# Kernel tuning notes

Measured on AMD Instinct MI355X. Metric: run time of the kernel, lower is better.

Reference implementation:

```python
import jax, jax.numpy as jnp
import numpy as np

DN = ('NCHW', 'OIHW', 'NCHW')

def _conv(x, w, pad):
    return jax.lax.conv_general_dilated(x, w, (1, 1), [(pad, pad), (pad, pad)], dimension_numbers=DN)

def setup_inputs() -> dict:
    key = jax.random.key(0)
    ks = jax.random.split(key, 6)
    B, Cin, Csh, H, W = 4, 128, 64, 512, 512
    s = lambda fan: (2.0 / fan) ** 0.5  # kaiming-ish scale
    return {
        'feature': jax.random.normal(ks[0], (B, Cin, H, W), jnp.float32),
        'w_shared': jax.random.normal(ks[1], (Csh, Cin, 3, 3), jnp.float32) * s(Cin * 9),
        'w_cls': jax.random.normal(ks[2], (2, Csh, 1, 1), jnp.float32) * s(Csh),
        'b_cls': jnp.zeros((2,), jnp.float32),
        'w_box': jax.random.normal(ks[3], (6, Csh, 1, 1), jnp.float32) * s(Csh),
        'b_box': jnp.zeros((6,), jnp.float32),
        'w_dir': jax.random.normal(ks[4], (8, Csh, 1, 1), jnp.float32) * s(Csh),
        'b_dir': jnp.zeros((8,), jnp.float32),
        'w_scr': jax.random.normal(ks[5], (4, Csh, 1, 1), jnp.float32) * s(Csh),
        'b_scr': jnp.zeros((4,), jnp.float32),
    }

def reference(feature, w_shared, w_cls, b_cls, w_box, b_box, w_dir, b_dir, w_scr, b_scr):
    # shared 3x3 conv (no bias) + ReLU -> [B, 64, H, W]
    x = jax.nn.relu(_conv(feature, w_shared, 1))
    bias = lambda b: b[None, :, None, None]
    cls = _conv(x, w_cls, 0) + bias(b_cls)                 # [B, n_cls+1, H, W]
    box = _conv(x, w_box, 0) + bias(b_box)                 # [B, 6, H, W]
    dr = _conv(x, w_dir, 0) + bias(b_dir)                  # [B, 8, H, W]
    scr = jax.nn.sigmoid(_conv(x, w_scr, 0) + bias(b_scr)) # sigmoid_keys=['scr']
    return jnp.concatenate([cls, box, dr, scr], axis=1)    # [B, 20, H, W]
```

## Files before the change

### kernel.cpp

```cpp
#include <hip/hip_runtime.h>
#include <cstdint>
#include <cstddef>


typedef __bf16 bf16x8 __attribute__((ext_vector_type(8)));
typedef float f32x16 __attribute__((ext_vector_type(16)));
typedef float f32x4v __attribute__((ext_vector_type(4)));
typedef float f32x2v __attribute__((ext_vector_type(2)));

__device__ __forceinline__ int swz(int s, int hw) {
    int lin = (s << 5) | (hw << 4);
    return lin ^ ((lin >> 1) & 0x10) ^ ((lin >> 2) & 0x60);
}

__global__ void prep_w_kernel(const float* __restrict__ w, __bf16* __restrict__ ws3) {
    int idx = blockIdx.x * 256 + threadIdx.x;
    if (idx >= 64 * 128 * 9) return;
    int tap = idx % 9;
    int cin = (idx / 9) % 128;
    int och = idx / (9 * 128);
    int hc = cin >> 4;
    int hw = (cin >> 3) & 1;
    int j  = cin & 7;
    int dst = (((hc * 9 + tap) * 2 + hw) * 64 + och) * 8 + j;
    ws3[dst] = (__bf16)w[idx];
}

#define A_OFF(p)  ((p) ? 16896 : 0)
#define B_OFF(p)  (33792 + ((p) ? 18432 : 0))

__global__ __launch_bounds__(256, 2)
void det_main_kernel(const float* __restrict__ feature,
                     const __bf16* __restrict__ ws3,
                     const float* __restrict__ w_cls, const float* __restrict__ b_cls,
                     const float* __restrict__ w_box, const float* __restrict__ b_box,
                     const float* __restrict__ w_dir, const float* __restrict__ b_dir,
                     const float* __restrict__ w_scr, const float* __restrict__ b_scr,
                     float* __restrict__ out) {
    __shared__ __align__(1024) char s_all[74880];

    const int tid  = threadIdx.x;
    const int lane = tid & 63;
    const int wave = tid >> 6;
    const int l31  = lane & 31;
    const int hw   = lane >> 5;
    const int wrow = wave >> 1;
    const int wcb  = (wave & 1) * 64;

    const int bid = blockIdx.x;
    const int wg  = (bid & 7) * 512 + (bid >> 3);
    const int ck  = wg >> 9;
    const int bz  = ck >> 1;
    const int rem = wg & 511;
    const int h0  = (rem >> 1) * 2;
    const int w0  = ((ck & 1) * 2 + (rem & 1)) * 128;
    const size_t CH = 512 * 512;

    const int m_hw  = tid & 1;
    const int m_q   = (tid >> 1) & 31;
    const int m_row = tid >> 6;
    const int m_h   = h0 - 1 + m_row;
    const bool m_ok = (unsigned)m_h < 512u;
    const float* m_base = feature + (size_t)(bz * 128 + m_hw * 8) * CH
                        + (size_t)(m_ok ? m_h : 0) * 512 + (w0 + 4 * m_q);

    const bool e_on = (tid & 1) == 0;
    const int e_idx = tid >> 1;
    const int e_ee  = (e_idx >> 6) & 1;
    const int e_row = (e_idx >> 4) & 3;
    const int e_cin = e_idx & 15;
    const int e_h   = h0 - 1 + e_row;
    const int e_w   = e_ee ? (w0 + 128) : (w0 - 2);
    const bool e_ok = ((unsigned)e_h < 512u) && ((unsigned)e_w < 511u);
    const float* e_base = feature + (size_t)(bz * 128 + e_cin) * CH
                        + (size_t)(e_ok ? e_h : 0) * 512 + (e_ok ? e_w : 0);

    {
        char* s_wc = s_all + 70656;
        float* s_bias = (float*)(s_all + 74752);
        int och = tid >> 3;
        int j8  = (tid & 7) * 8;
        float v[8];
        if (och < 20) {
            const float* src = (och < 2)  ? (w_cls + och * 64)
                             : (och < 8)  ? (w_box + (och - 2) * 64)
                             : (och < 16) ? (w_dir + (och - 8) * 64)
                                          : (w_scr + (och - 16) * 64);
            #pragma unroll
            for (int j = 0; j < 8; ++j) v[j] = src[j8 + j];
        } else {
            #pragma unroll
            for (int j = 0; j < 8; ++j) v[j] = 0.f;
        }
        bf16x8 wv;
        #pragma unroll
        for (int j = 0; j < 8; ++j) wv[j] = (__bf16)v[j];
        *(bf16x8*)(s_wc + och * 128 + ((j8 * 2) ^ ((och & 7) << 4))) = wv;
        if (tid < 32) {
            s_bias[tid] = (tid < 2)  ? b_cls[tid]
                        : (tid < 8)  ? b_box[tid - 2]
                        : (tid < 16) ? b_dir[tid - 8]
                        : (tid < 20) ? b_scr[tid - 16] : 0.f;
        }
    }

    f32x4v Ra[8], Rb[8];
    f32x2v Ea, Eb;

    auto issueA = [&](int hc, f32x4v (&R)[8], f32x2v& E) {
        const float* p = m_base + (size_t)(hc * 16) * CH;
        #pragma unroll
        for (int j = 0; j < 8; ++j) R[j] = *(const f32x4v*)(p + (size_t)j * CH);
        if (e_on) E = *(const f32x2v*)(e_base + (size_t)(hc * 16) * CH);
    };

    auto writeA = [&](int hc, f32x4v (&R)[8], f32x2v& E) {
        char* ab = s_all + A_OFF(hc & 1);
        #pragma unroll
        for (int k = 0; k < 4; ++k) {
            bf16x8 g;
            #pragma unroll
            for (int j = 0; j < 8; ++j) g[j] = (__bf16)(m_ok ? R[j][k] : 0.f);
            int s = 2 + 4 * m_q + k;
            *(bf16x8*)(ab + m_row * 4224 + swz(s, m_hw)) = g;
        }
        if (e_on) {
            char* b2 = ab + e_row * 4224 + (e_cin & 7) * 2;
            int s0 = e_ee ? 130 : 0;
            *(__bf16*)(b2 + swz(s0,     e_cin >> 3)) = (__bf16)(e_ok ? E[0] : 0.f);
            *(__bf16*)(b2 + swz(s0 + 1, e_cin >> 3)) = (__bf16)(e_ok ? E[1] : 0.f);
        }
    };

    auto issueB = [&](int hc) {
        char* bb = s_all + B_OFF(hc & 1);
        const char* src = (const char*)ws3 + hc * 18432;
        #pragma unroll
        for (int i = 0; i < 4; ++i) {
            int g0 = i * 256 + wave * 64;
            __builtin_amdgcn_global_load_lds(
                (const __attribute__((address_space(1))) void*)(src + (size_t)(g0 + lane) * 16),
                (__attribute__((address_space(3))) void*)(bb + g0 * 16), 16, 0, 0);
        }
        if (wave < 2) {
            int g0 = 1024 + wave * 64;
            __builtin_amdgcn_global_load_lds(
                (const __attribute__((address_space(1))) void*)(src + (size_t)(g0 + lane) * 16),
                (__attribute__((address_space(3))) void*)(bb + g0 * 16), 16, 0, 0);
        }
    };

    f32x16 zero16;
    #pragma unroll
    for (int e = 0; e < 16; ++e) zero16[e] = 0.f;
    f32x16 acc[2][2];
    acc[0][0] = zero16; acc[0][1] = zero16; acc[1][0] = zero16; acc[1][1] = zero16;

    auto mfma_phase = [&](int hc) {
        const char* ab = s_all + A_OFF(hc & 1);
        const char* bb = s_all + B_OFF(hc & 1);
        #pragma unroll
        for (int tap = 0; tap < 9; ++tap) {
            const int kh = tap / 3, kw = tap % 3;
            bf16x8 Bf0 = *(const bf16x8*)(bb + (size_t)((tap * 2 + hw) * 64 +      l31) * 16);
            bf16x8 Bf1 = *(const bf16x8*)(bb + (size_t)((tap * 2 + hw) * 64 + 32 + l31) * 16);
            bf16x8 Af0 = *(const bf16x8*)(ab + (wrow + kh) * 4224 + swz(wcb +      l31 + kw + 1, hw));
            bf16x8 Af1 = *(const bf16x8*)(ab + (wrow + kh) * 4224 + swz(wcb + 32 + l31 + kw + 1, hw));
            __builtin_amdgcn_s_setprio(1);
            acc[0][0] = __builtin_amdgcn_mfma_f32_32x32x16_bf16(Af0, Bf0, acc[0][0], 0, 0, 0);
            acc[0][1] = __builtin_amdgcn_mfma_f32_32x32x16_bf16(Af0, Bf1, acc[0][1], 0, 0, 0);
            acc[1][0] = __builtin_amdgcn_mfma_f32_32x32x16_bf16(Af1, Bf0, acc[1][0], 0, 0, 0);
            acc[1][1] = __builtin_amdgcn_mfma_f32_32x32x16_bf16(Af1, Bf1, acc[1][1], 0, 0, 0);
            __builtin_amdgcn_s_setprio(0);
        }
    };

    issueA(0, Ra, Ea);
    issueB(0);
    issueA(1, Rb, Eb);
    __builtin_amdgcn_sched_barrier(0);
    writeA(0, Ra, Ea);
    asm volatile("s_waitcnt vmcnt(9) lgkmcnt(0)" ::: "memory");
    __builtin_amdgcn_s_barrier();
    __builtin_amdgcn_sched_barrier(0);

    #pragma unroll 1
    for (int h = 0; h < 7; ++h) {
        issueB(h + 1);
        if (h < 6) {
            if (h & 1) issueA(h + 2, Rb, Eb); else issueA(h + 2, Ra, Ea);
        }
        __builtin_amdgcn_sched_barrier(0);
        mfma_phase(h);
        __builtin_amdgcn_sched_barrier(0);
        if (h & 1) writeA(h + 1, Ra, Ea); else writeA(h + 1, Rb, Eb);
        if (h < 6) {
            asm volatile("s_waitcnt vmcnt(9) lgkmcnt(0)" ::: "memory");
        } else {
            asm volatile("s_waitcnt vmcnt(0) lgkmcnt(0)" ::: "memory");
        }
        __builtin_amdgcn_s_barrier();
        __builtin_amdgcn_sched_barrier(0);
    }
    mfma_phase(7);

    __syncthreads();
    __bf16* X = (__bf16*)s_all;
    #pragma unroll
    for (int mt = 0; mt < 2; ++mt) {
        #pragma unroll
        for (int nt = 0; nt < 2; ++nt) {
            #pragma unroll
            for (int r = 0; r < 16; ++r) {
                float v = fmaxf(acc[mt][nt][r], 0.f);
                int mrow = (r & 3) + 8 * (r >> 2) + 4 * hw;
                int pxb  = wave * 64 + mt * 32 + mrow;
                int ch   = nt * 32 + l31;
                int off  = pxb * 128 + ((ch * 2) ^ ((pxb & 7) << 4));
                *(__bf16*)((char*)X + off) = (__bf16)v;
            }
        }
    }

    const char* s_wc = s_all + 70656;
    const float* s_bias = (const float*)(s_all + 74752);
    f32x16 acc2[2];
    acc2[0] = zero16; acc2[1] = zero16;
    #pragma unroll
    for (int ks = 0; ks < 4; ++ks) {
        int ch0 = ks * 16 + hw * 8;
        int offA = l31 * 128 + ((ch0 * 2) ^ ((l31 & 7) << 4));
        bf16x8 a2 = *(const bf16x8*)(s_wc + offA);
        #pragma unroll
        for (int nt = 0; nt < 2; ++nt) {
            int pxb  = wave * 64 + nt * 32 + l31;
            int offB = pxb * 128 + ((ch0 * 2) ^ ((pxb & 7) << 4));
            bf16x8 b2 = *(const bf16x8*)((const char*)X + offB);
            acc2[nt] = __builtin_amdgcn_mfma_f32_32x32x16_bf16(a2, b2, acc2[nt], 0, 0, 0);
        }
    }

    const int h = h0 + wrow;
    #pragma unroll
    for (int nt = 0; nt < 2; ++nt) {
        int wg2 = w0 + wcb + nt * 32 + l31;
        #pragma unroll
        for (int r = 0; r < 16; ++r) {
            int och = (r & 3) + 8 * (r >> 2) + 4 * hw;
            if (och < 20) {
                float v = acc2[nt][r] + s_bias[och];
                if (och >= 16) v = 1.f / (1.f + __expf(-v));
                out[(((size_t)bz * 20 + och) * 512 + h) * 512 + wg2] = v;
            }
        }
    }
}

extern "C" void kernel_launch(void* const* d_in, const int* in_sizes, int n_in,
                              void* d_out, int out_size, void* d_ws, size_t ws_size,
                              hipStream_t stream) {
    const float* feature  = (const float*)d_in[0];
    const float* w_shared = (const float*)d_in[1];
    const float* w_cls = (const float*)d_in[2];
    const float* b_cls = (const float*)d_in[3];
    const float* w_box = (const float*)d_in[4];
    const float* b_box = (const float*)d_in[5];
    const float* w_dir = (const float*)d_in[6];
    const float* b_dir = (const float*)d_in[7];
    const float* w_scr = (const float*)d_in[8];
    const float* b_scr = (const float*)d_in[9];
    float* out = (float*)d_out;
    __bf16* ws3 = (__bf16*)d_ws;

    prep_w_kernel<<<288, 256, 0, stream>>>(w_shared, ws3);

    det_main_kernel<<<4096, 256, 0, stream>>>(feature, ws3,
                                              w_cls, b_cls, w_box, b_box,
                                              w_dir, b_dir, w_scr, b_scr, out);
}
```

Measured before the change: 261.6 us.

## Enlarge output tile to 4 rows per block to cut halo reloads

```diff
diff --git a/kernel.cpp b/kernel.cpp
--- a/kernel.cpp
+++ b/kernel.cpp
@@ -4,12 +4,13 @@
 
 
 typedef __bf16 bf16x8 __attribute__((ext_vector_type(8)));
+typedef __bf16 bf16x4 __attribute__((ext_vector_type(4)));
 typedef float f32x16 __attribute__((ext_vector_type(16)));
 typedef float f32x4v __attribute__((ext_vector_type(4)));
 typedef float f32x2v __attribute__((ext_vector_type(2)));
 
-__device__ __forceinline__ int swz(int s, int hw) {
-    int lin = (s << 5) | (hw << 4);
+__device__ __forceinline__ int swz(int s, int o) {
+    int lin = (s << 5) | (o << 4);
     return lin ^ ((lin >> 1) & 0x10) ^ ((lin >> 2) & 0x60);
 }
 
@@ -26,8 +27,10 @@
     ws3[dst] = (__bf16)w[idx];
 }
 
-#define A_OFF(p)  ((p) ? 16896 : 0)
-#define B_OFF(p)  (33792 + ((p) ? 18432 : 0))
+#define A_OFF(p)  ((p) ? 25344 : 0)
+#define B_BASE    50688
+#define WC_BASE   69120
+#define BIAS_BASE 73216
 
 __global__ __launch_bounds__(256, 2)
 void det_main_kernel(const float* __restrict__ feature,
@@ -37,47 +40,55 @@
                      const float* __restrict__ w_dir, const float* __restrict__ b_dir,
                      const float* __restrict__ w_scr, const float* __restrict__ b_scr,
                      float* __restrict__ out) {
-    __shared__ __align__(1024) char s_all[74880];
+    __shared__ __align__(1024) char s_all[73344];
 
     const int tid  = threadIdx.x;
     const int lane = tid & 63;
     const int wave = tid >> 6;
     const int l31  = lane & 31;
     const int hw   = lane >> 5;
-    const int wrow = wave >> 1;
-    const int wcb  = (wave & 1) * 64;
+    const int wcb  = wave * 32;
 
     const int bid = blockIdx.x;
-    const int wg  = (bid & 7) * 512 + (bid >> 3);
-    const int ck  = wg >> 9;
+    const int wg  = (bid & 7) * 256 + (bid >> 3);
+    const int ck  = wg >> 8;
     const int bz  = ck >> 1;
-    const int rem = wg & 511;
-    const int h0  = (rem >> 1) * 2;
+    const int rem = wg & 255;
+    const int h0  = (rem >> 1) * 4;
     const int w0  = ((ck & 1) * 2 + (rem & 1)) * 128;
     const size_t CH = 512 * 512;
 
-    const int m_hw  = tid & 1;
-    const int m_q   = (tid >> 1) & 31;
-    const int m_row = tid >> 6;
-    const int m_h   = h0 - 1 + m_row;
-    const bool m_ok = (unsigned)m_h < 512u;
-    const float* m_base = feature + (size_t)(bz * 128 + m_hw * 8) * CH
-                        + (size_t)(m_ok ? m_h : 0) * 512 + (w0 + 4 * m_q);
-
-    const bool e_on = (tid & 1) == 0;
-    const int e_idx = tid >> 1;
-    const int e_ee  = (e_idx >> 6) & 1;
-    const int e_row = (e_idx >> 4) & 3;
-    const int e_cin = e_idx & 15;
-    const int e_h   = h0 - 1 + e_row;
-    const int e_w   = e_ee ? (w0 + 128) : (w0 - 2);
-    const bool e_ok = ((unsigned)e_h < 512u) && ((unsigned)e_w < 511u);
-    const float* e_base = feature + (size_t)(bz * 128 + e_cin) * CH
-                        + (size_t)(e_ok ? e_h : 0) * 512 + (e_ok ? e_w : 0);
+    const int t_r0 = tid >> 6;
+    const int t_q  = (tid >> 1) & 31;
+    const int t_o  = tid & 1;
+    const int m_h  = h0 - 1 + t_r0;
+    const bool m_ok = (m_h >= 0);
+    const float* m_base = feature + (size_t)(bz * 128 + t_o * 8) * CH
+                        + (size_t)(m_ok ? m_h : 0) * 512 + (w0 + 4 * t_q);
+    const int t_r1 = 4 + (tid >> 7);
+    const int rem1 = tid & 127;
+    const int t_hq = rem1 >> 2;
+    const int t_ho = (rem1 >> 1) & 1;
+    const int t_hh = rem1 & 1;
+    const int hh_h = h0 - 1 + t_r1;
+    const bool h_ok = (hh_h < 512);
+    const float* h_base = feature + (size_t)(bz * 128 + t_ho * 8 + t_hh * 4) * CH
+                        + (size_t)(h_ok ? hh_h : 0) * 512 + (w0 + 4 * t_hq);
+    const bool e_on  = tid < 192;
+    const int e_side = tid / 96;
+    const int e_rem  = tid % 96;
+    const int e_r    = e_rem >> 4;
+    const int e_c    = e_rem & 15;
+    const int e_h    = h0 - 1 + e_r;
+    const int e_col  = e_side ? (w0 + 128) : (w0 - 2);
+    const bool e_ok  = e_on && ((unsigned)e_h < 512u)
+                     && (e_side ? (w0 + 128 < 512) : (w0 > 0));
+    const float* e_base = feature + (size_t)(bz * 128 + e_c) * CH
+                        + (size_t)(e_ok ? e_h : 0) * 512 + (e_ok ? e_col : 0);
 
     {
-        char* s_wc = s_all + 70656;
-        float* s_bias = (float*)(s_all + 74752);
+        char* s_wc = s_all + WC_BASE;
+        float* s_bias = (float*)(s_all + BIAS_BASE);
         int och = tid >> 3;
         int j8  = (tid & 7) * 8;
         float v[8];
@@ -104,36 +115,45 @@
         }
     }
 
-    f32x4v Ra[8], Rb[8];
-    f32x2v Ea, Eb;
-
-    auto issueA = [&](int hc, f32x4v (&R)[8], f32x2v& E) {
+    f32x4v Rm[8];
+    f32x4v Rh[4];
+    f32x2v Re;
+
+    auto issueA = [&](int hc) {
         const float* p = m_base + (size_t)(hc * 16) * CH;
         #pragma unroll
-        for (int j = 0; j < 8; ++j) R[j] = *(const f32x4v*)(p + (size_t)j * CH);
-        if (e_on) E = *(const f32x2v*)(e_base + (size_t)(hc * 16) * CH);
+        for (int j = 0; j < 8; ++j) Rm[j] = *(const f32x4v*)(p + (size_t)j * CH);
+        const float* p2 = h_base + (size_t)(hc * 16) * CH;
+        #pragma unroll
+        for (int j = 0; j < 4; ++j) Rh[j] = *(const f32x4v*)(p2 + (size_t)j * CH);
+        if (e_on) Re = *(const f32x2v*)(e_base + (size_t)(hc * 16) * CH);
     };
 
-    auto writeA = [&](int hc, f32x4v (&R)[8], f32x2v& E) {
+    auto writeA = [&](int hc) {
         char* ab = s_all + A_OFF(hc & 1);
         #pragma unroll
         for (int k = 0; k < 4; ++k) {
             bf16x8 g;
             #pragma unroll
-            for (int j = 0; j < 8; ++j) g[j] = (__bf16)(m_ok ? R[j][k] : 0.f);
-            int s = 2 + 4 * m_q + k;
-            *(bf16x8*)(ab + m_row * 4224 + swz(s, m_hw)) = g;
+            for (int j = 0; j < 8; ++j) g[j] = (__bf16)(m_ok ? Rm[j][k] : 0.f);
+            *(bf16x8*)(ab + t_r0 * 4224 + swz(4 * t_q + 1 + k, t_o)) = g;
+        }
+        #pragma unroll
+        for (int k = 0; k < 4; ++k) {
+            bf16x4 g;
+            #pragma unroll
+            for (int j = 0; j < 4; ++j) g[j] = (__bf16)(h_ok ? Rh[j][k] : 0.f);
+            *(bf16x4*)(ab + t_r1 * 4224 + swz(4 * t_hq + 1 + k, t_ho) + t_hh * 8) = g;
         }
         if (e_on) {
-            char* b2 = ab + e_row * 4224 + (e_cin & 7) * 2;
-            int s0 = e_ee ? 130 : 0;
-            *(__bf16*)(b2 + swz(s0,     e_cin >> 3)) = (__bf16)(e_ok ? E[0] : 0.f);
-            *(__bf16*)(b2 + swz(s0 + 1, e_cin >> 3)) = (__bf16)(e_ok ? E[1] : 0.f);
+            float v = e_side ? Re[0] : Re[1];
+            *(__bf16*)(ab + e_r * 4224 + swz(e_side ? 129 : 0, e_c >> 3) + (e_c & 7) * 2)
+                = (__bf16)(e_ok ? v : 0.f);
         }
     };
 
     auto issueB = [&](int hc) {
-        char* bb = s_all + B_OFF(hc & 1);
+        char* bb = s_all + B_BASE;
         const char* src = (const char*)ws3 + hc * 18432;
         #pragma unroll
         for (int i = 0; i < 4; ++i) {
@@ -153,104 +173,105 @@
     f32x16 zero16;
     #pragma unroll
     for (int e = 0; e < 16; ++e) zero16[e] = 0.f;
-    f32x16 acc[2][2];
-    acc[0][0] = zero16; acc[0][1] = zero16; acc[1][0] = zero16; acc[1][1] = zero16;
+    f32x16 acc[4][2];
+    #pragma unroll
+    for (int mt = 0; mt < 4; ++mt) { acc[mt][0] = zero16; acc[mt][1] = zero16; }
 
     auto mfma_phase = [&](int hc) {
         const char* ab = s_all + A_OFF(hc & 1);
-        const char* bb = s_all + B_OFF(hc & 1);
+        const char* bb = s_all + B_BASE;
         #pragma unroll
         for (int tap = 0; tap < 9; ++tap) {
             const int kh = tap / 3, kw = tap % 3;
-            bf16x8 Bf0 = *(const bf16x8*)(bb + (size_t)((tap * 2 + hw) * 64 +      l31) * 16);
-            bf16x8 Bf1 = *(const bf16x8*)(bb + (size_t)((tap * 2 + hw) * 64 + 32 + l31) * 16);
-            bf16x8 Af0 = *(const bf16x8*)(ab + (wrow + kh) * 4224 + swz(wcb +      l31 + kw + 1, hw));
-            bf16x8 Af1 = *(const bf16x8*)(ab + (wrow + kh) * 4224 + swz(wcb + 32 + l31 + kw + 1, hw));
+            bf16x8 Bf[2];
+            #pragma unroll
+            for (int nt = 0; nt < 2; ++nt)
+                Bf[nt] = *(const bf16x8*)(bb + (size_t)((tap * 2 + hw) * 64 + nt * 32 + l31) * 16);
+            bf16x8 Af[4];
+            #pragma unroll
+            for (int mt = 0; mt < 4; ++mt)
+                Af[mt] = *(const bf16x8*)(ab + (mt + kh) * 4224 + swz(wcb + l31 + kw, hw));
             __builtin_amdgcn_s_setprio(1);
-            acc[0][0] = __builtin_amdgcn_mfma_f32_32x32x16_bf16(Af0, Bf0, acc[0][0], 0, 0, 0);
-            acc[0][1] = __builtin_amdgcn_mfma_f32_32x32x16_bf16(Af0, Bf1, acc[0][1], 0, 0, 0);
-            acc[1][0] = __builtin_amdgcn_mfma_f32_32x32x16_bf16(Af1, Bf0, acc[1][0], 0, 0, 0);
-            acc[1][1] = __builtin_amdgcn_mfma_f32_32x32x16_bf16(Af1, Bf1, acc[1][1], 0, 0, 0);
+            #pragma unroll
+            for (int mt = 0; mt < 4; ++mt) {
+                acc[mt][0] = __builtin_amdgcn_mfma_f32_32x32x16_bf16(Af[mt], Bf[0], acc[mt][0], 0, 0, 0);
+                acc[mt][1] = __builtin_amdgcn_mfma_f32_32x32x16_bf16(Af[mt], Bf[1], acc[mt][1], 0, 0, 0);
+            }
             __builtin_amdgcn_s_setprio(0);
         }
     };
 
-    issueA(0, Ra, Ea);
     issueB(0);
-    issueA(1, Rb, Eb);
+    issueA(0);
+    writeA(0);
+    issueA(1);
     __builtin_amdgcn_sched_barrier(0);
-    writeA(0, Ra, Ea);
-    asm volatile("s_waitcnt vmcnt(9) lgkmcnt(0)" ::: "memory");
+    asm volatile("s_waitcnt lgkmcnt(0)" ::: "memory");
     __builtin_amdgcn_s_barrier();
     __builtin_amdgcn_sched_barrier(0);
 
     #pragma unroll 1
-    for (int h = 0; h < 7; ++h) {
-        issueB(h + 1);
-        if (h < 6) {
-            if (h & 1) issueA(h + 2, Rb, Eb); else issueA(h + 2, Ra, Ea);
-        }
-        __builtin_amdgcn_sched_barrier(0);
+    for (int h = 0; h < 8; ++h) {
         mfma_phase(h);
         __builtin_amdgcn_sched_barrier(0);
-        if (h & 1) writeA(h + 1, Ra, Ea); else writeA(h + 1, Rb, Eb);
-        if (h < 6) {
-            asm volatile("s_waitcnt vmcnt(9) lgkmcnt(0)" ::: "memory");
-        } else {
-            asm volatile("s_waitcnt vmcnt(0) lgkmcnt(0)" ::: "memory");
-        }
         __builtin_amdgcn_s_barrier();
         __builtin_amdgcn_sched_barrier(0);
-    }
-    mfma_phase(7);
-
-    __syncthreads();
+        if (h == 7) break;
+        issueB(h + 1);
+        writeA(h + 1);
+        asm volatile("s_waitcnt vmcnt(0) lgkmcnt(0)" ::: "memory");
+        if (h < 6) issueA(h + 2);
+        __builtin_amdgcn_sched_barrier(0);
+        __builtin_amdgcn_s_barrier();
+        __builtin_amdgcn_sched_barrier(0);
+    }
+
     __bf16* X = (__bf16*)s_all;
     #pragma unroll
-    for (int mt = 0; mt < 2; ++mt) {
+    for (int mt = 0; mt < 4; ++mt) {
         #pragma unroll
         for (int nt = 0; nt < 2; ++nt) {
             #pragma unroll
             for (int r = 0; r < 16; ++r) {
                 float v = fmaxf(acc[mt][nt][r], 0.f);
                 int mrow = (r & 3) + 8 * (r >> 2) + 4 * hw;
-                int pxb  = wave * 64 + mt * 32 + mrow;
+                int px   = mt * 128 + wcb + mrow;
                 int ch   = nt * 32 + l31;
-                int off  = pxb * 128 + ((ch * 2) ^ ((pxb & 7) << 4));
+                int off  = px * 128 + ((ch * 2) ^ ((px & 7) << 4));
                 *(__bf16*)((char*)X + off) = (__bf16)v;
             }
         }
     }
 
-    const char* s_wc = s_all + 70656;
-    const float* s_bias = (const float*)(s_all + 74752);
-    f32x16 acc2[2];
-    acc2[0] = zero16; acc2[1] = zero16;
+    const char* s_wc = s_all + WC_BASE;
+    const float* s_bias = (const float*)(s_all + BIAS_BASE);
+    f32x16 acc2[4];
+    #pragma unroll
+    for (int pt = 0; pt < 4; ++pt) acc2[pt] = zero16;
     #pragma unroll
     for (int ks = 0; ks < 4; ++ks) {
         int ch0 = ks * 16 + hw * 8;
-        int offA = l31 * 128 + ((ch0 * 2) ^ ((l31 & 7) << 4));
-        bf16x8 a2 = *(const bf16x8*)(s_wc + offA);
-        #pragma unroll
-        for (int nt = 0; nt < 2; ++nt) {
-            int pxb  = wave * 64 + nt * 32 + l31;
-            int offB = pxb * 128 + ((ch0 * 2) ^ ((pxb & 7) << 4));
+        bf16x8 a2 = *(const bf16x8*)(s_wc + l31 * 128 + ((ch0 * 2) ^ ((l31 & 7) << 4)));
+        #pragma unroll
+        for (int pt = 0; pt < 4; ++pt) {
+            int px = pt * 128 + wcb + l31;
+            int offB = px * 128 + ((ch0 * 2) ^ ((px & 7) << 4));
             bf16x8 b2 = *(const bf16x8*)((const char*)X + offB);
-            acc2[nt] = __builtin_amdgcn_mfma_f32_32x32x16_bf16(a2, b2, acc2[nt], 0, 0, 0);
-        }
-    }
-
-    const int h = h0 + wrow;
-    #pragma unroll
-    for (int nt = 0; nt < 2; ++nt) {
-        int wg2 = w0 + wcb + nt * 32 + l31;
+            acc2[pt] = __builtin_amdgcn_mfma_f32_32x32x16_bf16(a2, b2, acc2[pt], 0, 0, 0);
+        }
+    }
+
+    #pragma unroll
+    for (int pt = 0; pt < 4; ++pt) {
+        int hrow = h0 + pt;
+        int wcol = w0 + wcb + l31;
         #pragma unroll
         for (int r = 0; r < 16; ++r) {
             int och = (r & 3) + 8 * (r >> 2) + 4 * hw;
             if (och < 20) {
-                float v = acc2[nt][r] + s_bias[och];
+                float v = acc2[pt][r] + s_bias[och];
                 if (och >= 16) v = 1.f / (1.f + __expf(-v));
-                out[(((size_t)bz * 20 + och) * 512 + h) * 512 + wg2] = v;
+                out[(((size_t)bz * 20 + och) * 512 + hrow) * 512 + wcol] = v;
             }
         }
     }
@@ -274,7 +295,7 @@
 
     prep_w_kernel<<<288, 256, 0, stream>>>(w_shared, ws3);
 
-    det_main_kernel<<<4096, 256, 0, stream>>>(feature, ws3,
+    det_main_kernel<<<2048, 256, 0, stream>>>(feature, ws3,
                                               w_cls, b_cls, w_box, b_box,
                                               w_dir, b_dir, w_scr, b_scr, out);
 }
```

Result: slower. 296.3 us (+13.2%).

## Pre-transpose feature to bf16 channel-octet layout and load conv tiles via direct-to-LDS

Applied to the files above, without the earlier changes.

```diff
diff --git a/kernel.cpp b/kernel.cpp
--- a/kernel.cpp
+++ b/kernel.cpp
@@ -4,14 +4,15 @@
 
 
 typedef __bf16 bf16x8 __attribute__((ext_vector_type(8)));
+typedef __bf16 bf16x4 __attribute__((ext_vector_type(4)));
 typedef float f32x16 __attribute__((ext_vector_type(16)));
 typedef float f32x4v __attribute__((ext_vector_type(4)));
 typedef float f32x2v __attribute__((ext_vector_type(2)));
 
-__device__ __forceinline__ int swz(int s, int hw) {
-    int lin = (s << 5) | (hw << 4);
-    return lin ^ ((lin >> 1) & 0x10) ^ ((lin >> 2) & 0x60);
-}
+#define CHW (512 * 512)
+#define ZB_OFF  147456
+#define FT_OFF  262144
+#define FT_BYTES 67108864ull
 
 __global__ void prep_w_kernel(const float* __restrict__ w, __bf16* __restrict__ ws3) {
     int idx = blockIdx.x * 256 + threadIdx.x;
@@ -26,19 +27,233 @@
     ws3[dst] = (__bf16)w[idx];
 }
 
+__global__ __launch_bounds__(256)
+void prep_t_kernel(const float* __restrict__ feature, __bf16* __restrict__ ft, int bz) {
+    const int b   = blockIdx.x;
+    const int oct = b & 15;
+    const int hp  = b >> 4;
+    const int tid = threadIdx.x;
+    const int h   = hp * 2 + (tid >> 7);
+    const int w4  = (tid & 127) * 4;
+    const float* src = feature + (size_t)(bz * 128 + oct * 8) * CHW + h * 512 + w4;
+    f32x4v R[8];
+    #pragma unroll
+    for (int j = 0; j < 8; ++j) R[j] = *(const f32x4v*)(src + (size_t)j * CHW);
+    #pragma unroll
+    for (int k = 0; k < 4; ++k) {
+        bf16x8 g;
+        #pragma unroll
+        for (int j = 0; j < 8; ++j) g[j] = (__bf16)R[j][k];
+        *(bf16x8*)(ft + ((size_t)(oct * 512 + h) * 512 + (w4 + k)) * 8) = g;
+    }
+}
+
+__global__ __launch_bounds__(512, 4)
+void det_main_t(const char* __restrict__ ft, const char* __restrict__ zbuf,
+                const __bf16* __restrict__ ws3,
+                const float* __restrict__ w_cls, const float* __restrict__ b_cls,
+                const float* __restrict__ w_box, const float* __restrict__ b_box,
+                const float* __restrict__ w_dir, const float* __restrict__ b_dir,
+                const float* __restrict__ w_scr, const float* __restrict__ b_scr,
+                float* __restrict__ out, int bz) {
+    __shared__ __align__(1024) char s_all[73344];
+
+    const int tid  = threadIdx.x;
+    const int lane = tid & 63;
+    const int wave = tid >> 6;
+    const int l31  = lane & 31;
+    const int hw   = lane >> 5;
+    const int wrow = wave >> 1;
+    const int wch  = wave & 1;
+
+    const int bid = blockIdx.x;
+    const int wg  = (bid & 7) * 64 + (bid >> 3);
+    const int w_t = wg >> 7;
+    const int h_t = wg & 127;
+    const int h0  = h_t * 4;
+    const int w0  = w_t * 128;
+
+    int a_lds[5]; const char* a_src[5]; int a_step[5];
+    #pragma unroll
+    for (int i = 0; i < 5; ++i) {
+        int e = wave * 5 + i; if (e >= 36) e -= 36;
+        int ro = e / 3, c3 = e - ro * 3;
+        int row = ro >> 1, oct = ro & 1;
+        int start = (c3 == 0) ? 0 : (c3 == 1) ? 64 : 66;
+        a_lds[i] = (row * 2 + oct) * 2112 + start * 16;
+        int hrow = h0 - 1 + row;
+        int wv   = w0 - 1 + start + lane;
+        bool ok = ((unsigned)hrow < 512u) && ((unsigned)wv < 512u);
+        long off = ((long)(oct * 512 + (ok ? hrow : 0)) * 512 + (ok ? wv : 0)) * 16;
+        a_src[i]  = ok ? (ft + off) : zbuf;
+        a_step[i] = ok ? (2 * CHW * 16) : 0;
+    }
+    int b_lds[3]; const char* b_src[3];
+    #pragma unroll
+    for (int i = 0; i < 3; ++i) {
+        int j = wave * 3 + i; if (j >= 18) j -= 18;
+        b_lds[i] = 50688 + j * 1024;
+        b_src[i] = (const char*)ws3 + j * 1024 + lane * 16;
+    }
+
+    auto issueA = [&](int hc, int buf) {
+        #pragma unroll
+        for (int i = 0; i < 5; ++i)
+            __builtin_amdgcn_global_load_lds(
+                (const __attribute__((address_space(1))) void*)(a_src[i] + (long)hc * a_step[i]),
+                (__attribute__((address_space(3))) void*)(s_all + buf * 25344 + a_lds[i]),
+                16, 0, 0);
+    };
+    auto issueB = [&](int hc) {
+        #pragma unroll
+        for (int i = 0; i < 3; ++i)
+            __builtin_amdgcn_global_load_lds(
+                (const __attribute__((address_space(1))) void*)(b_src[i] + hc * 18432),
+                (__attribute__((address_space(3))) void*)(s_all + b_lds[i]),
+                16, 0, 0);
+    };
+
+    if (tid < 256) {
+        char* s_wc = s_all + 69120;
+        int och = tid >> 3;
+        int j8  = (tid & 7) * 8;
+        float v[8];
+        if (och < 20) {
+            const float* src = (och < 2)  ? (w_cls + och * 64)
+                             : (och < 8)  ? (w_box + (och - 2) * 64)
+                             : (och < 16) ? (w_dir + (och - 8) * 64)
+                                          : (w_scr + (och - 16) * 64);
+            #pragma unroll
+            for (int j = 0; j < 8; ++j) v[j] = src[j8 + j];
+        } else {
+            #pragma unroll
+            for (int j = 0; j < 8; ++j) v[j] = 0.f;
+        }
+        bf16x8 wv;
+        #pragma unroll
+        for (int j = 0; j < 8; ++j) wv[j] = (__bf16)v[j];
+        *(bf16x8*)(s_wc + och * 128 + ((j8 * 2) ^ ((och & 7) << 4))) = wv;
+        if (tid < 32) {
+            float* s_bias = (float*)(s_all + 73216);
+            s_bias[tid] = (tid < 2)  ? b_cls[tid]
+                        : (tid < 8)  ? b_box[tid - 2]
+                        : (tid < 16) ? b_dir[tid - 8]
+                        : (tid < 20) ? b_scr[tid - 16] : 0.f;
+        }
+    }
+
+    f32x16 zero16;
+    #pragma unroll
+    for (int e = 0; e < 16; ++e) zero16[e] = 0.f;
+    f32x16 acc[2][2];
+    acc[0][0] = zero16; acc[0][1] = zero16; acc[1][0] = zero16; acc[1][1] = zero16;
+
+    auto mfma_phase = [&](int buf) {
+        const char* ab = s_all + buf * 25344 + wrow * 4224 + hw * 2112
+                       + (wch * 64 + l31) * 16;
+        const char* bb = s_all + 50688 + hw * 1024 + l31 * 16;
+        #pragma unroll
+        for (int tap = 0; tap < 9; ++tap) {
+            const int kh = tap / 3, kw = tap % 3;
+            bf16x8 Bf0 = *(const bf16x8*)(bb + tap * 2048);
+            bf16x8 Bf1 = *(const bf16x8*)(bb + tap * 2048 + 512);
+            bf16x8 Af0 = *(const bf16x8*)(ab + kh * 4224 + kw * 16);
+            bf16x8 Af1 = *(const bf16x8*)(ab + kh * 4224 + kw * 16 + 512);
+            __builtin_amdgcn_s_setprio(1);
+            acc[0][0] = __builtin_amdgcn_mfma_f32_32x32x16_bf16(Af0, Bf0, acc[0][0], 0, 0, 0);
+            acc[0][1] = __builtin_amdgcn_mfma_f32_32x32x16_bf16(Af0, Bf1, acc[0][1], 0, 0, 0);
+            acc[1][0] = __builtin_amdgcn_mfma_f32_32x32x16_bf16(Af1, Bf0, acc[1][0], 0, 0, 0);
+            acc[1][1] = __builtin_amdgcn_mfma_f32_32x32x16_bf16(Af1, Bf1, acc[1][1], 0, 0, 0);
+            __builtin_amdgcn_s_setprio(0);
+        }
+    };
+
+    issueA(0, 0);
+    issueB(0);
+    issueA(1, 1);
+    asm volatile("s_waitcnt vmcnt(5) lgkmcnt(0)" ::: "memory");
+    __builtin_amdgcn_s_barrier();
+    __builtin_amdgcn_sched_barrier(0);
+
+    #pragma unroll 1
+    for (int h = 0; h < 8; ++h) {
+        mfma_phase(h & 1);
+        __builtin_amdgcn_sched_barrier(0);
+        __builtin_amdgcn_s_barrier();
+        __builtin_amdgcn_sched_barrier(0);
+        if (h == 7) break;
+        issueB(h + 1);
+        if (h < 6) issueA(h + 2, h & 1);
+        if (h < 6) asm volatile("s_waitcnt vmcnt(5)" ::: "memory");
+        else       asm volatile("s_waitcnt vmcnt(0)" ::: "memory");
+        __builtin_amdgcn_s_barrier();
+        __builtin_amdgcn_sched_barrier(0);
+    }
+
+    __bf16* X = (__bf16*)s_all;
+    #pragma unroll
+    for (int mt = 0; mt < 2; ++mt) {
+        #pragma unroll
+        for (int nt = 0; nt < 2; ++nt) {
+            #pragma unroll
+            for (int r = 0; r < 16; ++r) {
+                float v = fmaxf(acc[mt][nt][r], 0.f);
+                int mrow = (r & 3) + 8 * (r >> 2) + 4 * hw;
+                int px   = wrow * 128 + wch * 64 + mt * 32 + mrow;
+                int chn  = nt * 32 + l31;
+                *(__bf16*)((char*)X + px * 128 + ((chn * 2) ^ ((px & 7) << 4))) = (__bf16)v;
+            }
+        }
+    }
+
+    const char* s_wc = s_all + 69120;
+    const float* s_bias = (const float*)(s_all + 73216);
+    f32x16 acc2[2];
+    acc2[0] = zero16; acc2[1] = zero16;
+    #pragma unroll
+    for (int ks = 0; ks < 4; ++ks) {
+        int ch0 = ks * 16 + hw * 8;
+        bf16x8 a2 = *(const bf16x8*)(s_wc + l31 * 128 + ((ch0 * 2) ^ ((l31 & 7) << 4)));
+        #pragma unroll
+        for (int pt = 0; pt < 2; ++pt) {
+            int px = wave * 64 + pt * 32 + l31;
+            bf16x8 b2 = *(const bf16x8*)((const char*)X + px * 128 + ((ch0 * 2) ^ ((px & 7) << 4)));
+            acc2[pt] = __builtin_amdgcn_mfma_f32_32x32x16_bf16(a2, b2, acc2[pt], 0, 0, 0);
+        }
+    }
+
+    const int hrow = h0 + wrow;
+    #pragma unroll
+    for (int pt = 0; pt < 2; ++pt) {
+        int wcol = w0 + wch * 64 + pt * 32 + l31;
+        #pragma unroll
+        for (int r = 0; r < 16; ++r) {
+            int och = (r & 3) + 8 * (r >> 2) + 4 * hw;
+            if (och < 20) {
+                float v = acc2[pt][r] + s_bias[och];
+                if (och >= 16) v = 1.f / (1.f + __expf(-v));
+                out[(((size_t)bz * 20 + och) * 512 + hrow) * 512 + wcol] = v;
+            }
+        }
+    }
+}
+
+__device__ __forceinline__ int swz(int s, int o) {
+    int lin = (s << 5) | (o << 4);
+    return lin ^ ((lin >> 1) & 0x10) ^ ((lin >> 2) & 0x60);
+}
 #define A_OFF(p)  ((p) ? 16896 : 0)
 #define B_OFF(p)  (33792 + ((p) ? 18432 : 0))
 
 __global__ __launch_bounds__(256, 2)
-void det_main_kernel(const float* __restrict__ feature,
-                     const __bf16* __restrict__ ws3,
-                     const float* __restrict__ w_cls, const float* __restrict__ b_cls,
-                     const float* __restrict__ w_box, const float* __restrict__ b_box,
-                     const float* __restrict__ w_dir, const float* __restrict__ b_dir,
-                     const float* __restrict__ w_scr, const float* __restrict__ b_scr,
-                     float* __restrict__ out) {
+void det_main_fb(const float* __restrict__ feature,
+                 const __bf16* __restrict__ ws3,
+                 const float* __restrict__ w_cls, const float* __restrict__ b_cls,
+                 const float* __restrict__ w_box, const float* __restrict__ b_box,
+                 const float* __restrict__ w_dir, const float* __restrict__ b_dir,
+                 const float* __restrict__ w_scr, const float* __restrict__ b_scr,
+                 float* __restrict__ out) {
     __shared__ __align__(1024) char s_all[74880];
-
     const int tid  = threadIdx.x;
     const int lane = tid & 63;
     const int wave = tid >> 6;
@@ -46,7 +261,6 @@
     const int hw   = lane >> 5;
     const int wrow = wave >> 1;
     const int wcb  = (wave & 1) * 64;
-
     const int bid = blockIdx.x;
     const int wg  = (bid & 7) * 512 + (bid >> 3);
     const int ck  = wg >> 9;
@@ -54,16 +268,13 @@
     const int rem = wg & 511;
     const int h0  = (rem >> 1) * 2;
     const int w0  = ((ck & 1) * 2 + (rem & 1)) * 128;
-    const size_t CH = 512 * 512;
-
     const int m_hw  = tid & 1;
     const int m_q   = (tid >> 1) & 31;
     const int m_row = tid >> 6;
     const int m_h   = h0 - 1 + m_row;
     const bool m_ok = (unsigned)m_h < 512u;
-    const float* m_base = feature + (size_t)(bz * 128 + m_hw * 8) * CH
+    const float* m_base = feature + (size_t)(bz * 128 + m_hw * 8) * CHW
                         + (size_t)(m_ok ? m_h : 0) * 512 + (w0 + 4 * m_q);
-
     const bool e_on = (tid & 1) == 0;
     const int e_idx = tid >> 1;
     const int e_ee  = (e_idx >> 6) & 1;
@@ -72,9 +283,8 @@
     const int e_h   = h0 - 1 + e_row;
     const int e_w   = e_ee ? (w0 + 128) : (w0 - 2);
     const bool e_ok = ((unsigned)e_h < 512u) && ((unsigned)e_w < 511u);
-    const float* e_base = feature + (size_t)(bz * 128 + e_cin) * CH
+    const float* e_base = feature + (size_t)(bz * 128 + e_cin) * CHW
                         + (size_t)(e_ok ? e_h : 0) * 512 + (e_ok ? e_w : 0);
-
     {
         char* s_wc = s_all + 70656;
         float* s_bias = (float*)(s_all + 74752);
@@ -103,17 +313,14 @@
                         : (tid < 20) ? b_scr[tid - 16] : 0.f;
         }
     }
-
     f32x4v Ra[8], Rb[8];
     f32x2v Ea, Eb;
-
     auto issueA = [&](int hc, f32x4v (&R)[8], f32x2v& E) {
-        const float* p = m_base + (size_t)(hc * 16) * CH;
-        #pragma unroll
-        for (int j = 0; j < 8; ++j) R[j] = *(const f32x4v*)(p + (size_t)j * CH);
-        if (e_on) E = *(const f32x2v*)(e_base + (size_t)(hc * 16) * CH);
-    };
-
+        const float* p = m_base + (size_t)(hc * 16) * CHW;
+        #pragma unroll
+        for (int j = 0; j < 8; ++j) R[j] = *(const f32x4v*)(p + (size_t)j * CHW);
+        if (e_on) E = *(const f32x2v*)(e_base + (size_t)(hc * 16) * CHW);
+    };
     auto writeA = [&](int hc, f32x4v (&R)[8], f32x2v& E) {
         char* ab = s_all + A_OFF(hc & 1);
         #pragma unroll
@@ -121,8 +328,7 @@
             bf16x8 g;
             #pragma unroll
             for (int j = 0; j < 8; ++j) g[j] = (__bf16)(m_ok ? R[j][k] : 0.f);
-            int s = 2 + 4 * m_q + k;
-            *(bf16x8*)(ab + m_row * 4224 + swz(s, m_hw)) = g;
+            *(bf16x8*)(ab + m_row * 4224 + swz(2 + 4 * m_q + k, m_hw)) = g;
         }
         if (e_on) {
             char* b2 = ab + e_row * 4224 + (e_cin & 7) * 2;
@@ -131,7 +337,6 @@
             *(__bf16*)(b2 + swz(s0 + 1, e_cin >> 3)) = (__bf16)(e_ok ? E[1] : 0.f);
         }
     };
-
     auto issueB = [&](int hc) {
         char* bb = s_all + B_OFF(hc & 1);
         const char* src = (const char*)ws3 + hc * 18432;
@@ -149,13 +354,11 @@
                 (__attribute__((address_space(3))) void*)(bb + g0 * 16), 16, 0, 0);
         }
     };
-
     f32x16 zero16;
     #pragma unroll
     for (int e = 0; e < 16; ++e) zero16[e] = 0.f;
     f32x16 acc[2][2];
     acc[0][0] = zero16; acc[0][1] = zero16; acc[1][0] = zero16; acc[1][1] = zero16;
-
     auto mfma_phase = [&](int hc) {
         const char* ab = s_all + A_OFF(hc & 1);
         const char* bb = s_all + B_OFF(hc & 1);
@@ -174,7 +377,6 @@
             __builtin_amdgcn_s_setprio(0);
         }
     };
-
     issueA(0, Ra, Ea);
     issueB(0);
     issueA(1, Rb, Eb);
@@ -183,45 +385,34 @@
     asm volatile("s_waitcnt vmcnt(9) lgkmcnt(0)" ::: "memory");
     __builtin_amdgcn_s_barrier();
     __builtin_amdgcn_sched_barrier(0);
-
     #pragma unroll 1
     for (int h = 0; h < 7; ++h) {
         issueB(h + 1);
-        if (h < 6) {
-            if (h & 1) issueA(h + 2, Rb, Eb); else issueA(h + 2, Ra, Ea);
-        }
+        if (h < 6) { if (h & 1) issueA(h + 2, Rb, Eb); else issueA(h + 2, Ra, Ea); }
         __builtin_amdgcn_sched_barrier(0);
         mfma_phase(h);
         __builtin_amdgcn_sched_barrier(0);
         if (h & 1) writeA(h + 1, Ra, Ea); else writeA(h + 1, Rb, Eb);
-        if (h < 6) {
-            asm volatile("s_waitcnt vmcnt(9) lgkmcnt(0)" ::: "memory");
-        } else {
-            asm volatile("s_waitcnt vmcnt(0) lgkmcnt(0)" ::: "memory");
-        }
+        if (h < 6) asm volatile("s_waitcnt vmcnt(9) lgkmcnt(0)" ::: "memory");
+        else       asm volatile("s_waitcnt vmcnt(0) lgkmcnt(0)" ::: "memory");
         __builtin_amdgcn_s_barrier();
         __builtin_amdgcn_sched_barrier(0);
     }
     mfma_phase(7);
-
     __syncthreads();
     __bf16* X = (__bf16*)s_all;
     #pragma unroll
-    for (int mt = 0; mt < 2; ++mt) {
-        #pragma unroll
-        for (int nt = 0; nt < 2; ++nt) {
+    for (int mt = 0; mt < 2; ++mt)
+        #pragma unroll
+        for (int nt = 0; nt < 2; ++nt)
             #pragma unroll
             for (int r = 0; r < 16; ++r) {
                 float v = fmaxf(acc[mt][nt][r], 0.f);
                 int mrow = (r & 3) + 8 * (r >> 2) + 4 * hw;
                 int pxb  = wave * 64 + mt * 32 + mrow;
-                int ch   = nt * 32 + l31;
-                int off  = pxb * 128 + ((ch * 2) ^ ((pxb & 7) << 4));
-                *(__bf16*)((char*)X + off) = (__bf16)v;
+                int chn  = nt * 32 + l31;
+                *(__bf16*)((char*)X + pxb * 128 + ((chn * 2) ^ ((pxb & 7) << 4))) = (__bf16)v;
             }
-        }
-    }
-
     const char* s_wc = s_all + 70656;
     const float* s_bias = (const float*)(s_all + 74752);
     f32x16 acc2[2];
@@ -229,17 +420,14 @@
     #pragma unroll
     for (int ks = 0; ks < 4; ++ks) {
         int ch0 = ks * 16 + hw * 8;
-        int offA = l31 * 128 + ((ch0 * 2) ^ ((l31 & 7) << 4));
-        bf16x8 a2 = *(const bf16x8*)(s_wc + offA);
+        bf16x8 a2 = *(const bf16x8*)(s_wc + l31 * 128 + ((ch0 * 2) ^ ((l31 & 7) << 4)));
         #pragma unroll
         for (int nt = 0; nt < 2; ++nt) {
             int pxb  = wave * 64 + nt * 32 + l31;
-            int offB = pxb * 128 + ((ch0 * 2) ^ ((pxb & 7) << 4));
-            bf16x8 b2 = *(const bf16x8*)((const char*)X + offB);
+            bf16x8 b2 = *(const bf16x8*)((const char*)X + pxb * 128 + ((ch0 * 2) ^ ((pxb & 7) << 4)));
             acc2[nt] = __builtin_amdgcn_mfma_f32_32x32x16_bf16(a2, b2, acc2[nt], 0, 0, 0);
         }
     }
-
     const int h = h0 + wrow;
     #pragma unroll
     for (int nt = 0; nt < 2; ++nt) {
@@ -274,7 +462,20 @@
 
     prep_w_kernel<<<288, 256, 0, stream>>>(w_shared, ws3);
 
-    det_main_kernel<<<4096, 256, 0, stream>>>(feature, ws3,
+    const size_t need = (size_t)FT_OFF + FT_BYTES;
+    if (ws_size >= need) {
+        hipMemsetAsync((char*)d_ws + ZB_OFF, 0, 64, stream);
+        char* ft = (char*)d_ws + FT_OFF;
+        const char* zbuf = (const char*)d_ws + ZB_OFF;
+        for (int bz = 0; bz < 4; ++bz) {
+            prep_t_kernel<<<4096, 256, 0, stream>>>(feature, (__bf16*)ft, bz);
+            det_main_t<<<512, 512, 0, stream>>>(ft, zbuf, ws3,
+                                                w_cls, b_cls, w_box, b_box,
+                                                w_dir, b_dir, w_scr, b_scr, out, bz);
+        }
+    } else {
+        det_main_fb<<<4096, 256, 0, stream>>>(feature, ws3,
                                               w_cls, b_cls, w_box, b_box,
                                               w_dir, b_dir, w_scr, b_scr, out);
-}
+    }
+}
```

Measured after the change: 346.2 us. 1.32x slower.

## Single-buffer weights and registers to fit three workgroups per CU

Applied to the files above, without the earlier changes.

```diff
diff --git a/kernel.cpp b/kernel.cpp
--- a/kernel.cpp
+++ b/kernel.cpp
@@ -8,8 +8,10 @@
 typedef float f32x4v __attribute__((ext_vector_type(4)));
 typedef float f32x2v __attribute__((ext_vector_type(2)));
 
-__device__ __forceinline__ int swz(int s, int hw) {
-    int lin = (s << 5) | (hw << 4);
+#define CHW (512 * 512)
+
+__device__ __forceinline__ int swz(int s, int o) {
+    int lin = (s << 5) | (o << 4);
     return lin ^ ((lin >> 1) & 0x10) ^ ((lin >> 2) & 0x60);
 }
 
@@ -27,9 +29,11 @@
 }
 
 #define A_OFF(p)  ((p) ? 16896 : 0)
-#define B_OFF(p)  (33792 + ((p) ? 18432 : 0))
-
-__global__ __launch_bounds__(256, 2)
+#define B_BASE    33792
+#define WC_BASE   33792
+#define BIAS_BASE 37888
+
+__global__ __launch_bounds__(256, 3)
 void det_main_kernel(const float* __restrict__ feature,
                      const __bf16* __restrict__ ws3,
                      const float* __restrict__ w_cls, const float* __restrict__ b_cls,
@@ -37,7 +41,7 @@
                      const float* __restrict__ w_dir, const float* __restrict__ b_dir,
                      const float* __restrict__ w_scr, const float* __restrict__ b_scr,
                      float* __restrict__ out) {
-    __shared__ __align__(1024) char s_all[74880];
+    __shared__ __align__(1024) char s_all[52224];
 
     const int tid  = threadIdx.x;
     const int lane = tid & 63;
@@ -54,16 +58,14 @@
     const int rem = wg & 511;
     const int h0  = (rem >> 1) * 2;
     const int w0  = ((ck & 1) * 2 + (rem & 1)) * 128;
-    const size_t CH = 512 * 512;
 
     const int m_hw  = tid & 1;
     const int m_q   = (tid >> 1) & 31;
     const int m_row = tid >> 6;
     const int m_h   = h0 - 1 + m_row;
     const bool m_ok = (unsigned)m_h < 512u;
-    const float* m_base = feature + (size_t)(bz * 128 + m_hw * 8) * CH
+    const float* m_base = feature + (size_t)(bz * 128 + m_hw * 8) * CHW
                         + (size_t)(m_ok ? m_h : 0) * 512 + (w0 + 4 * m_q);
-
     const bool e_on = (tid & 1) == 0;
     const int e_idx = tid >> 1;
     const int e_ee  = (e_idx >> 6) & 1;
@@ -72,57 +74,27 @@
     const int e_h   = h0 - 1 + e_row;
     const int e_w   = e_ee ? (w0 + 128) : (w0 - 2);
     const bool e_ok = ((unsigned)e_h < 512u) && ((unsigned)e_w < 511u);
-    const float* e_base = feature + (size_t)(bz * 128 + e_cin) * CH
+    const float* e_base = feature + (size_t)(bz * 128 + e_cin) * CHW
                         + (size_t)(e_ok ? e_h : 0) * 512 + (e_ok ? e_w : 0);
 
-    {
-        char* s_wc = s_all + 70656;
-        float* s_bias = (float*)(s_all + 74752);
-        int och = tid >> 3;
-        int j8  = (tid & 7) * 8;
-        float v[8];
-        if (och < 20) {
-            const float* src = (och < 2)  ? (w_cls + och * 64)
-                             : (och < 8)  ? (w_box + (och - 2) * 64)
-                             : (och < 16) ? (w_dir + (och - 8) * 64)
-                                          : (w_scr + (och - 16) * 64);
-            #pragma unroll
-            for (int j = 0; j < 8; ++j) v[j] = src[j8 + j];
-        } else {
-            #pragma unroll
-            for (int j = 0; j < 8; ++j) v[j] = 0.f;
-        }
-        bf16x8 wv;
-        #pragma unroll
-        for (int j = 0; j < 8; ++j) wv[j] = (__bf16)v[j];
-        *(bf16x8*)(s_wc + och * 128 + ((j8 * 2) ^ ((och & 7) << 4))) = wv;
-        if (tid < 32) {
-            s_bias[tid] = (tid < 2)  ? b_cls[tid]
-                        : (tid < 8)  ? b_box[tid - 2]
-                        : (tid < 16) ? b_dir[tid - 8]
-                        : (tid < 20) ? b_scr[tid - 16] : 0.f;
-        }
-    }
-
-    f32x4v Ra[8], Rb[8];
-    f32x2v Ea, Eb;
-
-    auto issueA = [&](int hc, f32x4v (&R)[8], f32x2v& E) {
-        const float* p = m_base + (size_t)(hc * 16) * CH;
-        #pragma unroll
-        for (int j = 0; j < 8; ++j) R[j] = *(const f32x4v*)(p + (size_t)j * CH);
-        if (e_on) E = *(const f32x2v*)(e_base + (size_t)(hc * 16) * CH);
-    };
-
-    auto writeA = [&](int hc, f32x4v (&R)[8], f32x2v& E) {
+    f32x4v R[8];
+    f32x2v E;
+
+    auto issueA = [&](int hc) {
+        const float* p = m_base + (size_t)(hc * 16) * CHW;
+        #pragma unroll
+        for (int j = 0; j < 8; ++j) R[j] = *(const f32x4v*)(p + (size_t)j * CHW);
+        if (e_on) E = *(const f32x2v*)(e_base + (size_t)(hc * 16) * CHW);
+    };
+
+    auto writeA = [&](int hc) {
         char* ab = s_all + A_OFF(hc & 1);
         #pragma unroll
         for (int k = 0; k < 4; ++k) {
             bf16x8 g;
             #pragma unroll
             for (int j = 0; j < 8; ++j) g[j] = (__bf16)(m_ok ? R[j][k] : 0.f);
-            int s = 2 + 4 * m_q + k;
-            *(bf16x8*)(ab + m_row * 4224 + swz(s, m_hw)) = g;
+            *(bf16x8*)(ab + m_row * 4224 + swz(2 + 4 * m_q + k, m_hw)) = g;
         }
         if (e_on) {
             char* b2 = ab + e_row * 4224 + (e_cin & 7) * 2;
@@ -133,7 +105,7 @@
     };
 
     auto issueB = [&](int hc) {
-        char* bb = s_all + B_OFF(hc & 1);
+        char* bb = s_all + B_BASE;
         const char* src = (const char*)ws3 + hc * 18432;
         #pragma unroll
         for (int i = 0; i < 4; ++i) {
@@ -158,7 +130,7 @@
 
     auto mfma_phase = [&](int hc) {
         const char* ab = s_all + A_OFF(hc & 1);
-        const char* bb = s_all + B_OFF(hc & 1);
+        const char* bb = s_all + B_BASE;
         #pragma unroll
         for (int tap = 0; tap < 9; ++tap) {
             const int kh = tap / 3, kw = tap % 3;
@@ -175,36 +147,31 @@
         }
     };
 
-    issueA(0, Ra, Ea);
     issueB(0);
-    issueA(1, Rb, Eb);
+    issueA(0);
+    writeA(0);
+    issueA(1);
     __builtin_amdgcn_sched_barrier(0);
-    writeA(0, Ra, Ea);
     asm volatile("s_waitcnt vmcnt(9) lgkmcnt(0)" ::: "memory");
     __builtin_amdgcn_s_barrier();
     __builtin_amdgcn_sched_barrier(0);
 
     #pragma unroll 1
-    for (int h = 0; h < 7; ++h) {
-        issueB(h + 1);
-        if (h < 6) {
-            if (h & 1) issueA(h + 2, Rb, Eb); else issueA(h + 2, Ra, Ea);
-        }
-        __builtin_amdgcn_sched_barrier(0);
+    for (int h = 0; h < 8; ++h) {
         mfma_phase(h);
         __builtin_amdgcn_sched_barrier(0);
-        if (h & 1) writeA(h + 1, Ra, Ea); else writeA(h + 1, Rb, Eb);
-        if (h < 6) {
-            asm volatile("s_waitcnt vmcnt(9) lgkmcnt(0)" ::: "memory");
-        } else {
-            asm volatile("s_waitcnt vmcnt(0) lgkmcnt(0)" ::: "memory");
-        }
         __builtin_amdgcn_s_barrier();
         __builtin_amdgcn_sched_barrier(0);
-    }
-    mfma_phase(7);
-
-    __syncthreads();
+        if (h == 7) break;
+        issueB(h + 1);
+        writeA(h + 1);
+        if (h < 6) issueA(h + 2);
+        if (h < 6) asm volatile("s_waitcnt vmcnt(9) lgkmcnt(0)" ::: "memory");
+        else       asm volatile("s_waitcnt vmcnt(0) lgkmcnt(0)" ::: "memory");
+        __builtin_amdgcn_s_barrier();
+        __builtin_amdgcn_sched_barrier(0);
+    }
+
     __bf16* X = (__bf16*)s_all;
     #pragma unroll
     for (int mt = 0; mt < 2; ++mt) {
@@ -215,27 +182,54 @@
                 float v = fmaxf(acc[mt][nt][r], 0.f);
                 int mrow = (r & 3) + 8 * (r >> 2) + 4 * hw;
                 int pxb  = wave * 64 + mt * 32 + mrow;
-                int ch   = nt * 32 + l31;
-                int off  = pxb * 128 + ((ch * 2) ^ ((pxb & 7) << 4));
-                *(__bf16*)((char*)X + off) = (__bf16)v;
+                int chn  = nt * 32 + l31;
+                *(__bf16*)((char*)X + pxb * 128 + ((chn * 2) ^ ((pxb & 7) << 4))) = (__bf16)v;
             }
         }
     }
 
-    const char* s_wc = s_all + 70656;
-    const float* s_bias = (const float*)(s_all + 74752);
+    {
+        char* s_wc = s_all + WC_BASE;
+        float* s_bias = (float*)(s_all + BIAS_BASE);
+        int och = tid >> 3;
+        int j8  = (tid & 7) * 8;
+        float v[8];
+        if (och < 20) {
+            const float* src = (och < 2)  ? (w_cls + och * 64)
+                             : (och < 8)  ? (w_box + (och - 2) * 64)
+                             : (och < 16) ? (w_dir + (och - 8) * 64)
+                                          : (w_scr + (och - 16) * 64);
+            #pragma unroll
+            for (int j = 0; j < 8; ++j) v[j] = src[j8 + j];
+        } else {
+            #pragma unroll
+            for (int j = 0; j < 8; ++j) v[j] = 0.f;
+        }
+        bf16x8 wv;
+        #pragma unroll
+        for (int j = 0; j < 8; ++j) wv[j] = (__bf16)v[j];
+        *(bf16x8*)(s_wc + och * 128 + ((j8 * 2) ^ ((och & 7) << 4))) = wv;
+        if (tid < 32) {
+            s_bias[tid] = (tid < 2)  ? b_cls[tid]
+                        : (tid < 8)  ? b_box[tid - 2]
+                        : (tid < 16) ? b_dir[tid - 8]
+                        : (tid < 20) ? b_scr[tid - 16] : 0.f;
+        }
+    }
+    __syncthreads();
+
+    const char* s_wc = s_all + WC_BASE;
+    const float* s_bias = (const float*)(s_all + BIAS_BASE);
     f32x16 acc2[2];
     acc2[0] = zero16; acc2[1] = zero16;
     #pragma unroll
     for (int ks = 0; ks < 4; ++ks) {
         int ch0 = ks * 16 + hw * 8;
-        int offA = l31 * 128 + ((ch0 * 2) ^ ((l31 & 7) << 4));
-        bf16x8 a2 = *(const bf16x8*)(s_wc + offA);
+        bf16x8 a2 = *(const bf16x8*)(s_wc + l31 * 128 + ((ch0 * 2) ^ ((l31 & 7) << 4)));
         #pragma unroll
         for (int nt = 0; nt < 2; ++nt) {
-            int pxb  = wave * 64 + nt * 32 + l31;
-            int offB = pxb * 128 + ((ch0 * 2) ^ ((pxb & 7) << 4));
-            bf16x8 b2 = *(const bf16x8*)((const char*)X + offB);
+            int pxb = wave * 64 + nt * 32 + l31;
+            bf16x8 b2 = *(const bf16x8*)((const char*)X + pxb * 128 + ((ch0 * 2) ^ ((pxb & 7) << 4)));
             acc2[nt] = __builtin_amdgcn_mfma_f32_32x32x16_bf16(a2, b2, acc2[nt], 0, 0, 0);
         }
     }
```

Result: faster. 227.8 us (-12.9%).
